# Kernel optimization log

Hardware: AMD Instinct MI355X
Metric: run time of the kernel (lower is better)

The kernel has to match this reference:

```python
import jax, jax.numpy as jnp
import numpy as np

EMBED_DIM = 256
NUM_HEADS = 8
HEAD_DIM = EMBED_DIM // NUM_HEADS


def setup_inputs() -> dict:
    key0 = jax.random.key(0)
    ks = jax.random.split(key0, 12)
    B, T, S, E = 4, 256, 16384, EMBED_DIM
    inv = 1.0 / np.sqrt(E)
    inputs = {
        "query": jax.random.normal(ks[0], (B, T, E), dtype=jnp.float32),
        "key": jax.random.normal(ks[1], (B, S, E), dtype=jnp.float32),
        "value": jax.random.normal(ks[2], (B, S, E), dtype=jnp.float32),
        "mask": jax.random.uniform(ks[3], (B, T, S), dtype=jnp.float32),
        # nn.MultiheadAttention in-projection (split into q/k/v parts) and out-projection
        "Wq": jax.random.uniform(ks[4], (E, E), jnp.float32, -inv, inv),
        "bq": jnp.zeros((E,), jnp.float32),
        "Wk": jax.random.uniform(ks[5], (E, E), jnp.float32, -inv, inv),
        "bk": jnp.zeros((E,), jnp.float32),
        "Wv": jax.random.uniform(ks[6], (E, E), jnp.float32, -inv, inv),
        "bv": jnp.zeros((E,), jnp.float32),
        "Wo": jax.random.uniform(ks[7], (E, E), jnp.float32, -inv, inv),
        "bo": jnp.zeros((E,), jnp.float32),
        # fixed default scaling factors (num_heads must be 8)
        "scaling_factors": jnp.asarray([32.0, 32.0, 16.0, 16.0, 8.0, 8.0, 4.0, 4.0], jnp.float32),
    }
    return inputs


def reference(query, key, value, mask, Wq, bq, Wk, bk, Wv, bv, Wo, bo, scaling_factors):
    B, T, E = query.shape
    S = key.shape[1]
    H, D = NUM_HEADS, HEAD_DIM
    # input projections (torch Linear convention: x @ W.T + b)
    q = (query @ Wq.T + bq).reshape(B, T, H, D).transpose(0, 2, 1, 3)  # [B,H,T,D]
    k = (key @ Wk.T + bk).reshape(B, S, H, D).transpose(0, 2, 1, 3)    # [B,H,S,D]
    v = (value @ Wv.T + bv).reshape(B, S, H, D).transpose(0, 2, 1, 3)  # [B,H,S,D]
    scale = 1.0 / jnp.sqrt(jnp.asarray(D, query.dtype))
    scores = jnp.einsum("bhtd,bhsd->bhts", q * scale, k)               # [B,H,T,S]
    # per-head scaled soft mask added as attention bias
    bias = mask[:, None, :, :] * scaling_factors[None, :, None, None]  # [B,H,T,S]
    attn = jax.nn.softmax(scores + bias, axis=-1)
    out = jnp.einsum("bhts,bhsd->bhtd", attn, v)                       # [B,H,T,D]
    out = out.transpose(0, 2, 1, 3).reshape(B, T, E)
    return out @ Wo.T + bo
```

## Files before the change

kernel.cpp:

```cpp
#include <hip/hip_runtime.h>

#define B_ 4
#define T_ 256
#define S_ 16384
#define E_ 256
#define H_ 8
#define D_ 32

typedef _Float16 f16;
typedef _Float16 f16x2 __attribute__((ext_vector_type(2)));
typedef _Float16 f16x4 __attribute__((ext_vector_type(4)));
typedef _Float16 f16x8 __attribute__((ext_vector_type(8)));
typedef float f32x4 __attribute__((ext_vector_type(4)));

typedef const __attribute__((address_space(1))) void* gas_t;
typedef __attribute__((address_space(3))) void* las_t;

#define FENCE() asm volatile("" ::: "memory")

__device__ __forceinline__ void gload_lds16(const void* g, void* l) {
    __builtin_amdgcn_global_load_lds((gas_t)g, (las_t)l, 16, 0, 0);
}

__device__ __forceinline__ f16x2 cvt_pk_f16(float a, float b) {
    return __builtin_bit_cast(f16x2, __builtin_amdgcn_cvt_pkrtz(a, b));
}

__device__ __forceinline__ f16x8 pack8(float4 a, float4 b) {
    f16x2 p0 = cvt_pk_f16(a.x, a.y), p1 = cvt_pk_f16(a.z, a.w);
    f16x2 p2 = cvt_pk_f16(b.x, b.y), p3 = cvt_pk_f16(b.z, b.w);
    return (f16x8){p0[0], p0[1], p1[0], p1[1], p2[0], p2[1], p3[0], p3[1]};
}

#define LOG2E 1.4426950408889634f

__global__ void cvt_w2_kernel(const float* __restrict__ wa, const float* __restrict__ wb,
                              f16* __restrict__ oa, f16* __restrict__ ob) {
    int m = blockIdx.y;
    const float* src = m == 0 ? wa : wb;
    f16* dst = m == 0 ? oa : ob;
    int i = (blockIdx.x * 256 + threadIdx.x) * 4;
    float4 v = *(const float4*)(src + i);
    f16x4 h = {(f16)v.x, (f16)v.y, (f16)v.z, (f16)v.w};
    *(f16x4*)(dst + i) = h;
}

template <bool OUT16>
__device__ __forceinline__ void qproj32_body(
    f16* SMEM, const float* __restrict__ in, const float* __restrict__ w,
    const float* __restrict__ bias, void* __restrict__ outp, int bid, float oscale)
{
    f16 (*As)[264] = (f16(*)[264])SMEM;
    f16 (*Bs)[264] = (f16(*)[264])(SMEM + 32 * 264);
    int tid = threadIdx.x;
    int wq = tid >> 6, ln = tid & 63, g = ln >> 4, lc = ln & 15;
    int row0 = (bid & 31) * 32;
    int n0 = (bid >> 5) * 32;
    {
        int r = tid >> 3, q0 = (tid & 7) * 32;
        const float* ip = in + (size_t)(row0 + r) * 256 + q0;
        #pragma unroll
        for (int i = 0; i < 4; i++) {
            float4 v0 = *(const float4*)(ip + i * 8);
            float4 v1 = *(const float4*)(ip + i * 8 + 4);
            *(f16x8*)&As[r][q0 + i * 8] = pack8(v0, v1);
        }
        const float* wp = w + (size_t)(n0 + r) * 256 + q0;
        #pragma unroll
        for (int i = 0; i < 4; i++) {
            float4 v0 = *(const float4*)(wp + i * 8);
            float4 v1 = *(const float4*)(wp + i * 8 + 4);
            *(f16x8*)&Bs[r][q0 + i * 8] = pack8(v0, v1);
        }
    }
    __syncthreads();
    int mi = wq >> 1, ni = wq & 1;
    f32x4 acc = {0.f, 0.f, 0.f, 0.f};
    #pragma unroll
    for (int ks = 0; ks < 8; ks++) {
        f16x8 a = *(const f16x8*)&As[mi * 16 + lc][ks * 32 + g * 8];
        f16x8 bf = *(const f16x8*)&Bs[ni * 16 + lc][ks * 32 + g * 8];
        acc = __builtin_amdgcn_mfma_f32_16x16x32_f16(a, bf, acc, 0, 0, 0);
    }
    int n = n0 + ni * 16 + lc;
    float bv = bias[n];
    #pragma unroll
    for (int r = 0; r < 4; r++) {
        int row = row0 + mi * 16 + g * 4 + r;
        float val = (acc[r] + bv) * oscale;
        if (OUT16) ((f16*)outp)[(size_t)row * 256 + n] = (f16)val;
        else       ((float*)outp)[(size_t)row * 256 + n] = val;
    }
}

template <int MODE>
__device__ __forceinline__ void proj_body4(
    char* SMEM, const float* __restrict__ in, const f16* __restrict__ w16,
    const float* __restrict__ bias, f16* __restrict__ out, int bx, float oscale)
{
    f16 (*As)[64][40] = (f16(*)[64][40])SMEM;
    f16* Bs = (f16*)(SMEM + 10240);
    int tid = threadIdx.x;
    int wv = tid >> 6, ln = tid & 63, g = ln >> 4, lc = ln & 15;
    int row0 = bx * 64;

    f32x4 acc[4][4];
    #pragma unroll
    for (int i = 0; i < 4; i++)
        #pragma unroll
        for (int j = 0; j < 4; j++) acc[i][j] = (f32x4){0.f, 0.f, 0.f, 0.f};

    int am = tid >> 3, akq = (tid & 7) << 2;
    const float* abase = in + (size_t)(row0 + am) * 256 + akq;

    float4 Ar[2][2];
    auto issueA = [&](int t) {
        const float* p = abase + t * 32;
        Ar[t & 1][0] = *(const float4*)p;
        Ar[t & 1][1] = *(const float4*)(p + (size_t)32 * 256);
    };
    auto wrA = [&](int t) {
        float4 v0 = Ar[t & 1][0], v1 = Ar[t & 1][1];
        f16x4 h0 = {(f16)v0.x, (f16)v0.y, (f16)v0.z, (f16)v0.w};
        f16x4 h1 = {(f16)v1.x, (f16)v1.y, (f16)v1.z, (f16)v1.w};
        *(f16x4*)&As[t & 1][am][akq] = h0;
        *(f16x4*)&As[t & 1][am + 32][akq] = h1;
    };
    auto issueB = [&](int t) {
        int kb = t * 32;
        #pragma unroll
        for (int c4 = 0; c4 < 4; c4++) {
            int cc = wv * 4 + c4;
            int row = cc * 16 + (ln >> 2);
            int sj = (ln & 3) ^ ((row >> 1) & 3);
            gload_lds16(w16 + (size_t)row * 256 + kb + sj * 8,
                        (char*)Bs + (t & 1) * 16384 + cc * 1024);
        }
    };

    issueB(0);
    FENCE();
    issueA(0); issueA(1);
    FENCE();

    #pragma unroll
    for (int t = 0; t < 8; t++) {
        if (t < 7) { asm volatile("s_waitcnt vmcnt(2)" ::: "memory"); }
        else       { asm volatile("s_waitcnt vmcnt(0)" ::: "memory"); }
        wrA(t);
        asm volatile("s_waitcnt lgkmcnt(0)" ::: "memory");
        __builtin_amdgcn_s_barrier();
        FENCE();
        if (t + 1 < 8) { issueB(t + 1); FENCE(); }
        if (t + 2 < 8) { issueA(t + 2); FENCE(); }

        f16x8 af[4], bf[4];
        #pragma unroll
        for (int mi = 0; mi < 4; mi++) af[mi] = *(const f16x8*)&As[t & 1][mi * 16 + lc][g * 8];
        #pragma unroll
        for (int ni = 0; ni < 4; ni++) {
            int n = wv * 64 + ni * 16 + lc;
            bf[ni] = *(const f16x8*)&Bs[(t & 1) * 8192 + n * 32 + ((g ^ ((n >> 1) & 3)) << 3)];
        }
        #pragma unroll
        for (int mi = 0; mi < 4; mi++)
            #pragma unroll
            for (int ni = 0; ni < 4; ni++)
                acc[mi][ni] = __builtin_amdgcn_mfma_f32_16x16x32_f16(af[mi], bf[ni], acc[mi][ni], 0, 0, 0);
    }

    if (MODE == 1) {
        #pragma unroll
        for (int ni = 0; ni < 4; ni++) {
            int n = wv * 64 + ni * 16 + lc;
            float bv = bias[n];
            #pragma unroll
            for (int mi = 0; mi < 4; mi++) {
                #pragma unroll
                for (int r = 0; r < 4; r++) {
                    int row = row0 + mi * 16 + g * 4 + r;
                    out[(size_t)row * 256 + n] = (f16)((acc[mi][ni][r] + bv) * oscale);
                }
            }
        }
    } else {
        f16* TR = (f16*)SMEM;
        __syncthreads();
        #pragma unroll
        for (int ni = 0; ni < 4; ni++) {
            int n = wv * 64 + ni * 16 + lc;
            float bv = bias[n];
            #pragma unroll
            for (int mi = 0; mi < 4; mi++) {
                f16x4 hv;
                #pragma unroll
                for (int r = 0; r < 4; r++) hv[r] = (f16)((acc[mi][ni][r] + bv) * oscale);
                *(f16x4*)&TR[n * 68 + mi * 16 + g * 4] = hv;
            }
        }
        __syncthreads();
        int bb = row0 >> 14, sbase = row0 & 16383;
        #pragma unroll
        for (int p = 0; p < 4; p++) {
            int n = p * 64 + wv * 16 + (ln >> 2);
            int sc = (ln & 3) * 16;
            f16x8 v0 = *(const f16x8*)&TR[n * 68 + sc];
            f16x8 v1 = *(const f16x8*)&TR[n * 68 + sc + 8];
            f16* op = out + ((size_t)(bb * 256 + n)) * 16384 + sbase + sc;
            *(f16x8*)op = v0;
            *(f16x8*)(op + 8) = v1;
        }
    }
}

__global__ __launch_bounds__(256, 3) void proj_fused4(
    const float* __restrict__ query, const float* __restrict__ key, const float* __restrict__ value,
    const float* __restrict__ Wq, const f16* __restrict__ Wk16, const f16* __restrict__ Wv16,
    const float* __restrict__ bq, const float* __restrict__ bk, const float* __restrict__ bv,
    f16* __restrict__ q16, f16* __restrict__ k16, f16* __restrict__ v16T, float qscale)
{
    __shared__ __align__(16) char SMEM[43008];
    int bx = blockIdx.x;
    if (bx < 1024) {
        proj_body4<1>(SMEM, key, Wk16, bk, k16, bx, 1.0f);
    } else if (bx < 2048) {
        proj_body4<2>(SMEM, value, Wv16, bv, v16T, bx - 1024, 1.0f);
    } else {
        qproj32_body<true>((f16*)SMEM, query, Wq, bq, q16, bx - 2048, qscale);
    }
}

__global__ __launch_bounds__(256, 4) void out_proj(
    const float* __restrict__ in, const float* __restrict__ w,
    const float* __restrict__ bias, float* __restrict__ outp)
{
    __shared__ __align__(16) f16 SMEM[16896];
    qproj32_body<false>(SMEM, in, w, bias, outp, blockIdx.x + blockIdx.y * 32, 1.0f);
}

__global__ __launch_bounds__(1024, 4) void attn_kernel(
    const f16* __restrict__ q16,
    const f16* __restrict__ k16,
    const f16* __restrict__ v16T,
    const float* __restrict__ mask,
    const float* __restrict__ scal,
    float* __restrict__ partO, float* __restrict__ partL)
{
    constexpr int ITERS = 16;
    __shared__ __align__(16) f16 KT[3][32 * 256];
    __shared__ __align__(16) f16 VT[3][256 * 32];
    __shared__ __align__(16) float MT[3][128 * 32];

    int raw = blockIdx.x;
    int th = raw >> 7, b = (raw >> 5) & 3, ck = raw & 31;
    int tid = threadIdx.x;
    int wv = tid >> 6;
    int h = wv & 7, tsub = wv >> 3;
    int ln = tid & 63, g = ln >> 4, lc = ln & 15;
    int t0 = th * 128, s0 = ck * 512;

    float sc_h = scal[h] * LOG2E;
    float negfix = -(sc_h + 4.0f);

    f16x8 qf[4];
    #pragma unroll
    for (int tl = 0; tl < 4; tl++) {
        const f16* qp = q16 + (size_t)(b * T_ + t0 + tsub * 64 + tl * 16 + lc) * E_ + h * 32 + g * 8;
        qf[tl] = *(const f16x8*)qp;
    }

    f32x4 oac[4][2];
    float l_part[4];
    #pragma unroll
    for (int tl = 0; tl < 4; tl++) {
        oac[tl][0] = (f32x4){0.f, 0.f, 0.f, 0.f};
        oac[tl][1] = (f32x4){0.f, 0.f, 0.f, 0.f};
        l_part[tl] = 0.f;
    }

    auto stage = [&](int it, int bufi) {
        int sg0 = s0 + it * 32;
        {
            int sl = wv * 2 + (ln >> 5);
            int slot = (sl ^ (sl >> 3)) & 7;
            int jc = (ln & 31) ^ slot;
            gload_lds16(k16 + (size_t)(b * S_ + sg0 + sl) * E_ + jc * 8,
                        (char*)&KT[bufi][0] + wv * 1024);
        }
        {
            int dl = wv * 16 + (ln >> 2);
            int srcj = (ln & 3) ^ ((dl >> 1) & 3);
            gload_lds16(v16T + (size_t)(b * E_ + dl) * S_ + sg0 + srcj * 8,
                        (char*)&VT[bufi][0] + wv * 1024);
        }
        {
            int r = ln >> 3;
            int sj = (ln & 7) ^ r;
            gload_lds16(mask + (size_t)(b * T_ + t0 + wv * 8 + r) * S_ + sg0 + sj * 4,
                        (char*)&MT[bufi][0] + wv * 1024);
        }
    };

    stage(0, 0);
    stage(1, 1);

    f32x4 zero4 = {0.f, 0.f, 0.f, 0.f};
    int ib = 0;

    #pragma unroll 1
    for (int it = 0; it < ITERS; it++) {
        if (it + 1 < ITERS) { asm volatile("s_waitcnt vmcnt(3)" ::: "memory"); }
        else                { asm volatile("s_waitcnt vmcnt(0)" ::: "memory"); }
        __builtin_amdgcn_s_barrier();
        FENCE();
        if (it + 2 < ITERS) {
            int wb = ib + 2; if (wb >= 3) wb -= 3;
            stage(it + 2, wb);
        }

        f16x8 kb[2];
        #pragma unroll
        for (int si = 0; si < 2; si++) {
            int sl = si * 16 + lc;
            int slot = (sl ^ (sl >> 3)) & 7;
            int j = (h * 4 + g) ^ slot;
            kb[si] = *(const f16x8*)((char*)&KT[ib][0] + sl * 512 + j * 16);
        }
        f16x4 va[2][2];
        #pragma unroll
        for (int si = 0; si < 2; si++) {
            #pragma unroll
            for (int ni = 0; ni < 2; ni++) {
                int d = h * 32 + ni * 16 + lc;
                int u = (si * 2 + (g >> 1)) ^ ((d >> 1) & 3);
                va[si][ni] = *(const f16x4*)((char*)&VT[ib][0] + d * 64 + u * 16 + (g & 1) * 8);
            }
        }

        #pragma unroll
        for (int tl = 0; tl < 4; tl++) {
            int t = tsub * 64 + tl * 16 + lc;
            const float4 mf0 = *(const float4*)((char*)&MT[ib][0] + t * 128 + (((g    ) ^ (t & 7)) << 4));
            const float4 mf1 = *(const float4*)((char*)&MT[ib][0] + t * 128 + (((4 + g) ^ (t & 7)) << 4));
            f32x4 st0 = __builtin_amdgcn_mfma_f32_16x16x32_f16(kb[0], qf[tl], zero4, 0, 0, 0);
            f32x4 st1 = __builtin_amdgcn_mfma_f32_16x16x32_f16(kb[1], qf[tl], zero4, 0, 0, 0);
            float p0 = __builtin_amdgcn_exp2f(st0[0] + __builtin_fmaf(mf0.x, sc_h, negfix));
            float p1 = __builtin_amdgcn_exp2f(st0[1] + __builtin_fmaf(mf0.y, sc_h, negfix));
            float p2 = __builtin_amdgcn_exp2f(st0[2] + __builtin_fmaf(mf0.z, sc_h, negfix));
            float p3 = __builtin_amdgcn_exp2f(st0[3] + __builtin_fmaf(mf0.w, sc_h, negfix));
            float p4 = __builtin_amdgcn_exp2f(st1[0] + __builtin_fmaf(mf1.x, sc_h, negfix));
            float p5 = __builtin_amdgcn_exp2f(st1[1] + __builtin_fmaf(mf1.y, sc_h, negfix));
            float p6 = __builtin_amdgcn_exp2f(st1[2] + __builtin_fmaf(mf1.z, sc_h, negfix));
            float p7 = __builtin_amdgcn_exp2f(st1[3] + __builtin_fmaf(mf1.w, sc_h, negfix));
            l_part[tl] += ((p0 + p1) + (p2 + p3)) + ((p4 + p5) + (p6 + p7));
            f16x2 c01 = cvt_pk_f16(p0, p1);
            f16x2 c23 = cvt_pk_f16(p2, p3);
            f16x2 c45 = cvt_pk_f16(p4, p5);
            f16x2 c67 = cvt_pk_f16(p6, p7);
            f16x4 pb0 = {c01[0], c01[1], c23[0], c23[1]};
            f16x4 pb1 = {c45[0], c45[1], c67[0], c67[1]};
            oac[tl][0] = __builtin_amdgcn_mfma_f32_16x16x16f16(va[0][0], pb0, oac[tl][0], 0, 0, 0);
            oac[tl][0] = __builtin_amdgcn_mfma_f32_16x16x16f16(va[1][0], pb1, oac[tl][0], 0, 0, 0);
            oac[tl][1] = __builtin_amdgcn_mfma_f32_16x16x16f16(va[0][1], pb0, oac[tl][1], 0, 0, 0);
            oac[tl][1] = __builtin_amdgcn_mfma_f32_16x16x16f16(va[1][1], pb1, oac[tl][1], 0, 0, 0);
        }
        ib++; if (ib >= 3) ib -= 3;
    }

    #pragma unroll
    for (int tl = 0; tl < 4; tl++) {
        float lv = l_part[tl];
        lv += __shfl_xor(lv, 16, 64);
        lv += __shfl_xor(lv, 32, 64);
        l_part[tl] = lv;
    }
    float* po = partO + (size_t)raw * 128 * 256;
    #pragma unroll
    for (int tl = 0; tl < 4; tl++) {
        #pragma unroll
        for (int ni = 0; ni < 2; ni++) {
            float4 o4 = {oac[tl][ni][0], oac[tl][ni][1], oac[tl][ni][2], oac[tl][ni][3]};
            *(float4*)(po + (size_t)(tsub * 64 + tl * 16 + lc) * 256 + h * 32 + ni * 16 + g * 4) = o4;
        }
    }
    if (g == 0) {
        float* pl = partL + (size_t)raw * 128 * 8;
        #pragma unroll
        for (int tl = 0; tl < 4; tl++) {
            int trow = tsub * 64 + tl * 16 + lc;
            pl[trow * 8 + h] = l_part[tl];
        }
    }
}

__global__ __launch_bounds__(256) void combine_kernel(
    const float* __restrict__ partO, const float* __restrict__ partL,
    float* __restrict__ attnO)
{
    int bid = blockIdx.x;
    int b = bid >> 8, t = bid & 255;
    int th = t >> 7, tl = t & 127;
    int tid = threadIdx.x;
    __shared__ float sl[32][8];
    {
        int ck = tid >> 3, hh = tid & 7;
        size_t blk = (size_t)(th * 128 + b * 32 + ck);
        sl[ck][hh] = partL[blk * 1024 + tl * 8 + hh];
    }
    __syncthreads();
    int h = tid >> 5;
    float L = 0.f;
    #pragma unroll 8
    for (int ck = 0; ck < 32; ck++) L += sl[ck][h];
    float acc = 0.f;
    #pragma unroll 4
    for (int ck = 0; ck < 32; ck++) {
        size_t blk = (size_t)(th * 128 + b * 32 + ck);
        acc += partO[blk * 32768 + (size_t)tl * 256 + tid];
    }
    attnO[(size_t)bid * 256 + tid] = acc / L;
}

extern "C" void kernel_launch(void* const* d_in, const int* in_sizes, int n_in,
                              void* d_out, int out_size, void* d_ws, size_t ws_size,
                              hipStream_t stream) {
    (void)in_sizes; (void)n_in; (void)out_size; (void)ws_size;
    const float* query = (const float*)d_in[0];
    const float* key   = (const float*)d_in[1];
    const float* value = (const float*)d_in[2];
    const float* mask  = (const float*)d_in[3];
    const float* Wq = (const float*)d_in[4];
    const float* bq = (const float*)d_in[5];
    const float* Wk = (const float*)d_in[6];
    const float* bk = (const float*)d_in[7];
    const float* Wv = (const float*)d_in[8];
    const float* bv = (const float*)d_in[9];
    const float* Wo = (const float*)d_in[10];
    const float* bo = (const float*)d_in[11];
    const float* scal = (const float*)d_in[12];

    char* ws = (char*)d_ws;
    f16* Wk16 = (f16*)(ws + 0);
    f16* Wv16 = (f16*)(ws + (1 << 17));
    f16* q16  = (f16*)(ws + (4 << 17));
    float* attnO = (float*)(ws + 1048576);
    f16* k16  = (f16*)(ws + 2097152);
    f16* v16T = (f16*)(ws + 35651584);
    float* partO = (float*)(ws + 69206016);
    float* partL = (float*)(ws + 103809024);

    cvt_w2_kernel<<<dim3(64, 2), 256, 0, stream>>>(Wk, Wv, Wk16, Wv16);

    const float qscale = 0.17677669529663687f * LOG2E;
    proj_fused4<<<2304, 256, 0, stream>>>(query, key, value, Wq, Wk16, Wv16,
                                          bq, bk, bv, q16, k16, v16T, qscale);

    attn_kernel<<<256, 1024, 0, stream>>>(q16, k16, v16T, mask, scal, partO, partL);
    combine_kernel<<<1024, 256, 0, stream>>>(partO, partL, attnO);

    out_proj<<<dim3(32, 8), 256, 0, stream>>>(attnO, Wo, bo, (float*)d_out);
}
```

Baseline: 127.3 us.

## Restructure K/V projection to 512-thread blocks with full A-tile preload

The K/V projection is rewritten to use 512-thread blocks. Each block loads the whole 64x256 fp32 input tile into LDS as f16 up front, and each wave owns a private 32-column slice of the weight tile, which removes the per-step block barrier and double buffering. The weight conversion and Q projection are merged into one pre-kernel, which removes a launch. The trade-off is more LDS per block and a single-buffered weight stream that can expose load latency.

```diff
diff --git a/kernel.cpp b/kernel.cpp
--- a/kernel.cpp
+++ b/kernel.cpp
@@ -33,17 +33,6 @@
 }
 
 #define LOG2E 1.4426950408889634f
-
-__global__ void cvt_w2_kernel(const float* __restrict__ wa, const float* __restrict__ wb,
-                              f16* __restrict__ oa, f16* __restrict__ ob) {
-    int m = blockIdx.y;
-    const float* src = m == 0 ? wa : wb;
-    f16* dst = m == 0 ? oa : ob;
-    int i = (blockIdx.x * 256 + threadIdx.x) * 4;
-    float4 v = *(const float4*)(src + i);
-    f16x4 h = {(f16)v.x, (f16)v.y, (f16)v.z, (f16)v.w};
-    *(f16x4*)(dst + i) = h;
-}
 
 template <bool OUT16>
 __device__ __forceinline__ void qproj32_body(
@@ -93,86 +82,99 @@
     }
 }
 
+__global__ __launch_bounds__(256) void pre_kernel(
+    const float* __restrict__ Wk, const float* __restrict__ Wv,
+    f16* __restrict__ Wk16, f16* __restrict__ Wv16,
+    const float* __restrict__ query, const float* __restrict__ Wq,
+    const float* __restrict__ bq, f16* __restrict__ q16, float qscale)
+{
+    __shared__ __align__(16) f16 SMEM[16896];
+    int bx = blockIdx.x;
+    if (bx < 128) {
+        const float* src = bx < 64 ? Wk : Wv;
+        f16* dst = bx < 64 ? Wk16 : Wv16;
+        int i = ((bx & 63) * 256 + threadIdx.x) * 4;
+        float4 v = *(const float4*)(src + i);
+        f16x4 h = {(f16)v.x, (f16)v.y, (f16)v.z, (f16)v.w};
+        *(f16x4*)(dst + i) = h;
+    } else {
+        qproj32_body<true>(SMEM, query, Wq, bq, q16, bx - 128, qscale);
+    }
+}
+
 template <int MODE>
-__device__ __forceinline__ void proj_body4(
+__device__ __forceinline__ void proj_body6(
     char* SMEM, const float* __restrict__ in, const f16* __restrict__ w16,
     const float* __restrict__ bias, f16* __restrict__ out, int bx, float oscale)
 {
-    f16 (*As)[64][40] = (f16(*)[64][40])SMEM;
-    f16* Bs = (f16*)(SMEM + 10240);
+    f16* As = (f16*)SMEM;
+    f16* Bs = (f16*)(SMEM + 33280);
     int tid = threadIdx.x;
-    int wv = tid >> 6, ln = tid & 63, g = ln >> 4, lc = ln & 15;
+    int wq = tid >> 6, ln = tid & 63, g = ln >> 4, lc = ln & 15;
     int row0 = bx * 64;
 
-    f32x4 acc[4][4];
-    #pragma unroll
-    for (int i = 0; i < 4; i++)
-        #pragma unroll
-        for (int j = 0; j < 4; j++) acc[i][j] = (f32x4){0.f, 0.f, 0.f, 0.f};
-
-    int am = tid >> 3, akq = (tid & 7) << 2;
-    const float* abase = in + (size_t)(row0 + am) * 256 + akq;
-
-    float4 Ar[2][2];
-    auto issueA = [&](int t) {
-        const float* p = abase + t * 32;
-        Ar[t & 1][0] = *(const float4*)p;
-        Ar[t & 1][1] = *(const float4*)(p + (size_t)32 * 256);
-    };
-    auto wrA = [&](int t) {
-        float4 v0 = Ar[t & 1][0], v1 = Ar[t & 1][1];
-        f16x4 h0 = {(f16)v0.x, (f16)v0.y, (f16)v0.z, (f16)v0.w};
-        f16x4 h1 = {(f16)v1.x, (f16)v1.y, (f16)v1.z, (f16)v1.w};
-        *(f16x4*)&As[t & 1][am][akq] = h0;
-        *(f16x4*)&As[t & 1][am + 32][akq] = h1;
-    };
     auto issueB = [&](int t) {
         int kb = t * 32;
         #pragma unroll
-        for (int c4 = 0; c4 < 4; c4++) {
-            int cc = wv * 4 + c4;
-            int row = cc * 16 + (ln >> 2);
+        for (int hh = 0; hh < 2; hh++) {
+            int row = wq * 32 + hh * 16 + (ln >> 2);
             int sj = (ln & 3) ^ ((row >> 1) & 3);
             gload_lds16(w16 + (size_t)row * 256 + kb + sj * 8,
-                        (char*)Bs + (t & 1) * 16384 + cc * 1024);
+                        (char*)Bs + (wq * 32 + hh * 16) * 64);
         }
     };
 
     issueB(0);
     FENCE();
-    issueA(0); issueA(1);
-    FENCE();
+    const float* ab = in + (size_t)row0 * 256;
+    f32x4 Ld[8];
+    #pragma unroll
+    for (int j = 0; j < 8; j++)
+        Ld[j] = *(const f32x4*)(ab + (size_t)j * 2048 + tid * 4);
+    asm volatile("s_waitcnt vmcnt(0)" ::: "memory");
+    #pragma unroll
+    for (int j = 0; j < 8; j++) {
+        int row = j * 8 + wq;
+        f16x4 h = {(f16)Ld[j][0], (f16)Ld[j][1], (f16)Ld[j][2], (f16)Ld[j][3]};
+        *(f16x4*)&As[row * 260 + ln * 4] = h;
+    }
+    __syncthreads();
+
+    f32x4 acc[4][2];
+    #pragma unroll
+    for (int i = 0; i < 4; i++) {
+        acc[i][0] = (f32x4){0.f, 0.f, 0.f, 0.f};
+        acc[i][1] = (f32x4){0.f, 0.f, 0.f, 0.f};
+    }
 
     #pragma unroll
     for (int t = 0; t < 8; t++) {
-        if (t < 7) { asm volatile("s_waitcnt vmcnt(2)" ::: "memory"); }
-        else       { asm volatile("s_waitcnt vmcnt(0)" ::: "memory"); }
-        wrA(t);
+        asm volatile("s_waitcnt vmcnt(0)" ::: "memory");
+        FENCE();
+        f16x8 bf[2];
+        #pragma unroll
+        for (int ni = 0; ni < 2; ni++) {
+            int n = wq * 32 + ni * 16 + lc;
+            bf[ni] = *(const f16x8*)&Bs[n * 32 + ((g ^ ((n >> 1) & 3)) << 3)];
+        }
         asm volatile("s_waitcnt lgkmcnt(0)" ::: "memory");
-        __builtin_amdgcn_s_barrier();
         FENCE();
         if (t + 1 < 8) { issueB(t + 1); FENCE(); }
-        if (t + 2 < 8) { issueA(t + 2); FENCE(); }
-
-        f16x8 af[4], bf[4];
-        #pragma unroll
-        for (int mi = 0; mi < 4; mi++) af[mi] = *(const f16x8*)&As[t & 1][mi * 16 + lc][g * 8];
-        #pragma unroll
-        for (int ni = 0; ni < 4; ni++) {
-            int n = wv * 64 + ni * 16 + lc;
-            bf[ni] = *(const f16x8*)&Bs[(t & 1) * 8192 + n * 32 + ((g ^ ((n >> 1) & 3)) << 3)];
-        }
+        f16x8 af[4];
         #pragma unroll
         for (int mi = 0; mi < 4; mi++)
-            #pragma unroll
-            for (int ni = 0; ni < 4; ni++)
-                acc[mi][ni] = __builtin_amdgcn_mfma_f32_16x16x32_f16(af[mi], bf[ni], acc[mi][ni], 0, 0, 0);
+            af[mi] = *(const f16x8*)&As[(mi * 16 + lc) * 260 + t * 32 + g * 8];
+        #pragma unroll
+        for (int mi = 0; mi < 4; mi++) {
+            acc[mi][0] = __builtin_amdgcn_mfma_f32_16x16x32_f16(af[mi], bf[0], acc[mi][0], 0, 0, 0);
+            acc[mi][1] = __builtin_amdgcn_mfma_f32_16x16x32_f16(af[mi], bf[1], acc[mi][1], 0, 0, 0);
+        }
     }
 
     if (MODE == 1) {
         #pragma unroll
-        for (int ni = 0; ni < 4; ni++) {
-            int n = wv * 64 + ni * 16 + lc;
+        for (int ni = 0; ni < 2; ni++) {
+            int n = wq * 32 + ni * 16 + lc;
             float bv = bias[n];
             #pragma unroll
             for (int mi = 0; mi < 4; mi++) {
@@ -187,8 +189,8 @@
         f16* TR = (f16*)SMEM;
         __syncthreads();
         #pragma unroll
-        for (int ni = 0; ni < 4; ni++) {
-            int n = wv * 64 + ni * 16 + lc;
+        for (int ni = 0; ni < 2; ni++) {
+            int n = wq * 32 + ni * 16 + lc;
             float bv = bias[n];
             #pragma unroll
             for (int mi = 0; mi < 4; mi++) {
@@ -201,8 +203,8 @@
         __syncthreads();
         int bb = row0 >> 14, sbase = row0 & 16383;
         #pragma unroll
-        for (int p = 0; p < 4; p++) {
-            int n = p * 64 + wv * 16 + (ln >> 2);
+        for (int p = 0; p < 2; p++) {
+            int n = p * 128 + wq * 16 + (ln >> 2);
             int sc = (ln & 3) * 16;
             f16x8 v0 = *(const f16x8*)&TR[n * 68 + sc];
             f16x8 v1 = *(const f16x8*)&TR[n * 68 + sc + 8];
@@ -213,21 +215,16 @@
     }
 }
 
-__global__ __launch_bounds__(256, 3) void proj_fused4(
-    const float* __restrict__ query, const float* __restrict__ key, const float* __restrict__ value,
-    const float* __restrict__ Wq, const f16* __restrict__ Wk16, const f16* __restrict__ Wv16,
-    const float* __restrict__ bq, const float* __restrict__ bk, const float* __restrict__ bv,
-    f16* __restrict__ q16, f16* __restrict__ k16, f16* __restrict__ v16T, float qscale)
-{
-    __shared__ __align__(16) char SMEM[43008];
+__global__ __launch_bounds__(512, 4) void proj_kv6(
+    const float* __restrict__ key, const float* __restrict__ value,
+    const f16* __restrict__ Wk16, const f16* __restrict__ Wv16,
+    const float* __restrict__ bk, const float* __restrict__ bv,
+    f16* __restrict__ k16, f16* __restrict__ v16T)
+{
+    __shared__ __align__(16) char SMEM[49664];
     int bx = blockIdx.x;
-    if (bx < 1024) {
-        proj_body4<1>(SMEM, key, Wk16, bk, k16, bx, 1.0f);
-    } else if (bx < 2048) {
-        proj_body4<2>(SMEM, value, Wv16, bv, v16T, bx - 1024, 1.0f);
-    } else {
-        qproj32_body<true>((f16*)SMEM, query, Wq, bq, q16, bx - 2048, qscale);
-    }
+    if (bx < 1024) proj_body6<1>(SMEM, key,   Wk16, bk, k16,  bx, 1.0f);
+    else           proj_body6<2>(SMEM, value, Wv16, bv, v16T, bx - 1024, 1.0f);
 }
 
 __global__ __launch_bounds__(256, 4) void out_proj(
@@ -449,11 +446,10 @@
     float* partO = (float*)(ws + 69206016);
     float* partL = (float*)(ws + 103809024);
 
-    cvt_w2_kernel<<<dim3(64, 2), 256, 0, stream>>>(Wk, Wv, Wk16, Wv16);
-
     const float qscale = 0.17677669529663687f * LOG2E;
-    proj_fused4<<<2304, 256, 0, stream>>>(query, key, value, Wq, Wk16, Wv16,
-                                          bq, bk, bv, q16, k16, v16T, qscale);
+    pre_kernel<<<384, 256, 0, stream>>>(Wk, Wv, Wk16, Wv16, query, Wq, bq, q16, qscale);
+
+    proj_kv6<<<2048, 512, 0, stream>>>(key, value, Wk16, Wv16, bk, bv, k16, v16T);
 
     attn_kernel<<<256, 1024, 0, stream>>>(q16, k16, v16T, mask, scal, partO, partL);
     combine_kernel<<<1024, 256, 0, stream>>>(partO, partL, attnO);
```

Result: slower. 145.2 us (+14.1%).

## Stream fp32 activations directly into LDS with triple-buffered async loads

Applied to the files above, without the earlier changes.

The K/V projection now loads the fp32 activation tiles straight into LDS with global_load_lds (XOR-swizzled) instead of going through registers, and converts to fp16 when reading fragments from LDS. Staging becomes a three-buffer ring with a two-tile lookahead and a single barrier per step. The aim is to remove register staging and the LDS write/lgkm wait from the critical path and overlap more memory traffic. In exchange, LDS use grows to 72KB and occupancy drops from 3 to 2 blocks per CU.

```diff
diff --git a/kernel.cpp b/kernel.cpp
--- a/kernel.cpp
+++ b/kernel.cpp
@@ -29,6 +29,12 @@
 __device__ __forceinline__ f16x8 pack8(float4 a, float4 b) {
     f16x2 p0 = cvt_pk_f16(a.x, a.y), p1 = cvt_pk_f16(a.z, a.w);
     f16x2 p2 = cvt_pk_f16(b.x, b.y), p3 = cvt_pk_f16(b.z, b.w);
+    return (f16x8){p0[0], p0[1], p1[0], p1[1], p2[0], p2[1], p3[0], p3[1]};
+}
+
+__device__ __forceinline__ f16x8 pack8v(f32x4 a, f32x4 b) {
+    f16x2 p0 = cvt_pk_f16(a[0], a[1]), p1 = cvt_pk_f16(a[2], a[3]);
+    f16x2 p2 = cvt_pk_f16(b[0], b[1]), p3 = cvt_pk_f16(b[2], b[3]);
     return (f16x8){p0[0], p0[1], p1[0], p1[1], p2[0], p2[1], p3[0], p3[1]};
 }
 
@@ -94,79 +100,77 @@
 }
 
 template <int MODE>
-__device__ __forceinline__ void proj_body4(
+__device__ __forceinline__ void proj_body7(
     char* SMEM, const float* __restrict__ in, const f16* __restrict__ w16,
     const float* __restrict__ bias, f16* __restrict__ out, int bx, float oscale)
 {
-    f16 (*As)[64][40] = (f16(*)[64][40])SMEM;
-    f16* Bs = (f16*)(SMEM + 10240);
+    char* Ab = SMEM;
+    char* Bb = SMEM + 24576;
     int tid = threadIdx.x;
     int wv = tid >> 6, ln = tid & 63, g = ln >> 4, lc = ln & 15;
     int row0 = bx * 64;
 
-    f32x4 acc[4][4];
-    #pragma unroll
-    for (int i = 0; i < 4; i++)
-        #pragma unroll
-        for (int j = 0; j < 4; j++) acc[i][j] = (f32x4){0.f, 0.f, 0.f, 0.f};
-
-    int am = tid >> 3, akq = (tid & 7) << 2;
-    const float* abase = in + (size_t)(row0 + am) * 256 + akq;
-
-    float4 Ar[2][2];
-    auto issueA = [&](int t) {
-        const float* p = abase + t * 32;
-        Ar[t & 1][0] = *(const float4*)p;
-        Ar[t & 1][1] = *(const float4*)(p + (size_t)32 * 256);
-    };
-    auto wrA = [&](int t) {
-        float4 v0 = Ar[t & 1][0], v1 = Ar[t & 1][1];
-        f16x4 h0 = {(f16)v0.x, (f16)v0.y, (f16)v0.z, (f16)v0.w};
-        f16x4 h1 = {(f16)v1.x, (f16)v1.y, (f16)v1.z, (f16)v1.w};
-        *(f16x4*)&As[t & 1][am][akq] = h0;
-        *(f16x4*)&As[t & 1][am + 32][akq] = h1;
-    };
-    auto issueB = [&](int t) {
-        int kb = t * 32;
+    auto stage = [&](int t, int buf) {
         #pragma unroll
         for (int c4 = 0; c4 < 4; c4++) {
             int cc = wv * 4 + c4;
             int row = cc * 16 + (ln >> 2);
             int sj = (ln & 3) ^ ((row >> 1) & 3);
-            gload_lds16(w16 + (size_t)row * 256 + kb + sj * 8,
-                        (char*)Bs + (t & 1) * 16384 + cc * 1024);
+            gload_lds16(w16 + (size_t)row * 256 + t * 32 + sj * 8,
+                        Bb + buf * 16384 + cc * 1024);
+        }
+        #pragma unroll
+        for (int q2 = 0; q2 < 2; q2++) {
+            int q = wv * 2 + q2;
+            int rl = ln >> 3;
+            int ssl = (ln & 7) ^ rl;
+            gload_lds16(in + (size_t)(row0 + q * 8 + rl) * 256 + t * 32 + ssl * 4,
+                        Ab + buf * 8192 + q * 1024);
         }
     };
 
-    issueB(0);
-    FENCE();
-    issueA(0); issueA(1);
-    FENCE();
-
-    #pragma unroll
+    f32x4 acc[4][4];
+    #pragma unroll
+    for (int i = 0; i < 4; i++)
+        #pragma unroll
+        for (int j = 0; j < 4; j++) acc[i][j] = (f32x4){0.f, 0.f, 0.f, 0.f};
+
+    stage(0, 0);
+    stage(1, 1);
+
+    int ib = 0;
+    #pragma unroll 1
     for (int t = 0; t < 8; t++) {
-        if (t < 7) { asm volatile("s_waitcnt vmcnt(2)" ::: "memory"); }
+        if (t < 7) { asm volatile("s_waitcnt vmcnt(6)" ::: "memory"); }
         else       { asm volatile("s_waitcnt vmcnt(0)" ::: "memory"); }
-        wrA(t);
-        asm volatile("s_waitcnt lgkmcnt(0)" ::: "memory");
         __builtin_amdgcn_s_barrier();
         FENCE();
-        if (t + 1 < 8) { issueB(t + 1); FENCE(); }
-        if (t + 2 < 8) { issueA(t + 2); FENCE(); }
+        if (t + 2 < 8) {
+            int wb = ib + 2; if (wb >= 3) wb -= 3;
+            stage(t + 2, wb);
+        }
 
         f16x8 af[4], bf[4];
         #pragma unroll
-        for (int mi = 0; mi < 4; mi++) af[mi] = *(const f16x8*)&As[t & 1][mi * 16 + lc][g * 8];
+        for (int mi = 0; mi < 4; mi++) {
+            int row = mi * 16 + lc;
+            int s0 = (2 * g) ^ (row & 7);
+            int s1 = (2 * g + 1) ^ (row & 7);
+            f32x4 lo = *(const f32x4*)(Ab + ib * 8192 + row * 128 + s0 * 16);
+            f32x4 hi = *(const f32x4*)(Ab + ib * 8192 + row * 128 + s1 * 16);
+            af[mi] = pack8v(lo, hi);
+        }
         #pragma unroll
         for (int ni = 0; ni < 4; ni++) {
             int n = wv * 64 + ni * 16 + lc;
-            bf[ni] = *(const f16x8*)&Bs[(t & 1) * 8192 + n * 32 + ((g ^ ((n >> 1) & 3)) << 3)];
+            bf[ni] = *(const f16x8*)(Bb + ib * 16384 + n * 64 + ((g ^ ((n >> 1) & 3)) << 4));
         }
         #pragma unroll
         for (int mi = 0; mi < 4; mi++)
             #pragma unroll
             for (int ni = 0; ni < 4; ni++)
                 acc[mi][ni] = __builtin_amdgcn_mfma_f32_16x16x32_f16(af[mi], bf[ni], acc[mi][ni], 0, 0, 0);
+        ib++; if (ib >= 3) ib -= 3;
     }
 
     if (MODE == 1) {
@@ -213,18 +217,18 @@
     }
 }
 
-__global__ __launch_bounds__(256, 3) void proj_fused4(
+__global__ __launch_bounds__(256, 2) void proj_fused7(
     const float* __restrict__ query, const float* __restrict__ key, const float* __restrict__ value,
     const float* __restrict__ Wq, const f16* __restrict__ Wk16, const f16* __restrict__ Wv16,
     const float* __restrict__ bq, const float* __restrict__ bk, const float* __restrict__ bv,
     f16* __restrict__ q16, f16* __restrict__ k16, f16* __restrict__ v16T, float qscale)
 {
-    __shared__ __align__(16) char SMEM[43008];
+    __shared__ __align__(16) char SMEM[73728];
     int bx = blockIdx.x;
     if (bx < 1024) {
-        proj_body4<1>(SMEM, key, Wk16, bk, k16, bx, 1.0f);
+        proj_body7<1>(SMEM, key, Wk16, bk, k16, bx, 1.0f);
     } else if (bx < 2048) {
-        proj_body4<2>(SMEM, value, Wv16, bv, v16T, bx - 1024, 1.0f);
+        proj_body7<2>(SMEM, value, Wv16, bv, v16T, bx - 1024, 1.0f);
     } else {
         qproj32_body<true>((f16*)SMEM, query, Wq, bq, q16, bx - 2048, qscale);
     }
@@ -452,7 +456,7 @@
     cvt_w2_kernel<<<dim3(64, 2), 256, 0, stream>>>(Wk, Wv, Wk16, Wv16);
 
     const float qscale = 0.17677669529663687f * LOG2E;
-    proj_fused4<<<2304, 256, 0, stream>>>(query, key, value, Wq, Wk16, Wv16,
+    proj_fused7<<<2304, 256, 0, stream>>>(query, key, value, Wq, Wk16, Wv16,
                                           bq, bk, bv, q16, k16, v16T, qscale);
 
     attn_kernel<<<256, 1024, 0, stream>>>(q16, k16, v16T, mask, scal, partO, partL);
```

Result: no change. 126.7 us, median of 2 (-0.4%).

## Enlarge K/V projection tiles to 128 rows and move Q projection into pre-kernel

Applied to the files above, without the earlier changes.

The K/V projection moves to a new 512-thread kernel that computes 128-row tiles with 8 waves, so each loaded weight tile serves twice as many rows. A-tile loads become contiguous 8-element chunks packed in one store. The K output is now staged through LDS for coalesced row writes. The Q projection is folded into the weight-conversion pre-kernel, which removes a launch and takes Q blocks out of the big projection grid. The costs are more LDS per block, lower occupancy (2 blocks of 512 threads), and extra barriers in the two-pass epilogue.

```diff
diff --git a/kernel.cpp b/kernel.cpp
--- a/kernel.cpp
+++ b/kernel.cpp
@@ -33,17 +33,6 @@
 }
 
 #define LOG2E 1.4426950408889634f
-
-__global__ void cvt_w2_kernel(const float* __restrict__ wa, const float* __restrict__ wb,
-                              f16* __restrict__ oa, f16* __restrict__ ob) {
-    int m = blockIdx.y;
-    const float* src = m == 0 ? wa : wb;
-    f16* dst = m == 0 ? oa : ob;
-    int i = (blockIdx.x * 256 + threadIdx.x) * 4;
-    float4 v = *(const float4*)(src + i);
-    f16x4 h = {(f16)v.x, (f16)v.y, (f16)v.z, (f16)v.w};
-    *(f16x4*)(dst + i) = h;
-}
 
 template <bool OUT16>
 __device__ __forceinline__ void qproj32_body(
@@ -93,16 +82,37 @@
     }
 }
 
+__global__ __launch_bounds__(256) void pre_kernel(
+    const float* __restrict__ Wk, const float* __restrict__ Wv,
+    f16* __restrict__ Wk16, f16* __restrict__ Wv16,
+    const float* __restrict__ query, const float* __restrict__ Wq,
+    const float* __restrict__ bq, f16* __restrict__ q16, float qscale)
+{
+    __shared__ __align__(16) f16 SMEM[16896];
+    int bx = blockIdx.x;
+    if (bx < 128) {
+        const float* src = bx < 64 ? Wk : Wv;
+        f16* dst = bx < 64 ? Wk16 : Wv16;
+        int i = ((bx & 63) * 256 + threadIdx.x) * 4;
+        float4 v = *(const float4*)(src + i);
+        f16x4 h = {(f16)v.x, (f16)v.y, (f16)v.z, (f16)v.w};
+        *(f16x4*)(dst + i) = h;
+    } else {
+        qproj32_body<true>(SMEM, query, Wq, bq, q16, bx - 128, qscale);
+    }
+}
+
 template <int MODE>
-__device__ __forceinline__ void proj_body4(
+__device__ __forceinline__ void proj8_body(
     char* SMEM, const float* __restrict__ in, const f16* __restrict__ w16,
-    const float* __restrict__ bias, f16* __restrict__ out, int bx, float oscale)
-{
-    f16 (*As)[64][40] = (f16(*)[64][40])SMEM;
-    f16* Bs = (f16*)(SMEM + 10240);
+    const float* __restrict__ bias, f16* __restrict__ out, int bx)
+{
+    f16 (*As)[128][40] = (f16(*)[128][40])SMEM;
+    f16* Bs = (f16*)(SMEM + 20480);
     int tid = threadIdx.x;
-    int wv = tid >> 6, ln = tid & 63, g = ln >> 4, lc = ln & 15;
-    int row0 = bx * 64;
+    int wq = tid >> 6, ln = tid & 63, g = ln >> 4, lc = ln & 15;
+    int mh = wq >> 2, nq = wq & 3;
+    int row0 = bx * 128;
 
     f32x4 acc[4][4];
     #pragma unroll
@@ -110,27 +120,23 @@
         #pragma unroll
         for (int j = 0; j < 4; j++) acc[i][j] = (f32x4){0.f, 0.f, 0.f, 0.f};
 
-    int am = tid >> 3, akq = (tid & 7) << 2;
+    int am = tid >> 2, akq = (tid & 3) << 3;
     const float* abase = in + (size_t)(row0 + am) * 256 + akq;
 
     float4 Ar[2][2];
     auto issueA = [&](int t) {
         const float* p = abase + t * 32;
         Ar[t & 1][0] = *(const float4*)p;
-        Ar[t & 1][1] = *(const float4*)(p + (size_t)32 * 256);
+        Ar[t & 1][1] = *(const float4*)(p + 4);
     };
     auto wrA = [&](int t) {
-        float4 v0 = Ar[t & 1][0], v1 = Ar[t & 1][1];
-        f16x4 h0 = {(f16)v0.x, (f16)v0.y, (f16)v0.z, (f16)v0.w};
-        f16x4 h1 = {(f16)v1.x, (f16)v1.y, (f16)v1.z, (f16)v1.w};
-        *(f16x4*)&As[t & 1][am][akq] = h0;
-        *(f16x4*)&As[t & 1][am + 32][akq] = h1;
+        *(f16x8*)&As[t & 1][am][akq] = pack8(Ar[t & 1][0], Ar[t & 1][1]);
     };
     auto issueB = [&](int t) {
         int kb = t * 32;
         #pragma unroll
-        for (int c4 = 0; c4 < 4; c4++) {
-            int cc = wv * 4 + c4;
+        for (int c2 = 0; c2 < 2; c2++) {
+            int cc = wq * 2 + c2;
             int row = cc * 16 + (ln >> 2);
             int sj = (ln & 3) ^ ((row >> 1) & 3);
             gload_lds16(w16 + (size_t)row * 256 + kb + sj * 8,
@@ -156,10 +162,11 @@
 
         f16x8 af[4], bf[4];
         #pragma unroll
-        for (int mi = 0; mi < 4; mi++) af[mi] = *(const f16x8*)&As[t & 1][mi * 16 + lc][g * 8];
+        for (int mi = 0; mi < 4; mi++)
+            af[mi] = *(const f16x8*)&As[t & 1][mh * 64 + mi * 16 + lc][g * 8];
         #pragma unroll
         for (int ni = 0; ni < 4; ni++) {
-            int n = wv * 64 + ni * 16 + lc;
+            int n = nq * 64 + ni * 16 + lc;
             bf[ni] = *(const f16x8*)&Bs[(t & 1) * 8192 + n * 32 + ((g ^ ((n >> 1) & 3)) << 3)];
         }
         #pragma unroll
@@ -170,64 +177,69 @@
     }
 
     if (MODE == 1) {
-        #pragma unroll
-        for (int ni = 0; ni < 4; ni++) {
-            int n = wv * 64 + ni * 16 + lc;
-            float bv = bias[n];
-            #pragma unroll
-            for (int mi = 0; mi < 4; mi++) {
+        f16 (*TR)[264] = (f16(*)[264])SMEM;
+        #pragma unroll
+        for (int p = 0; p < 2; p++) {
+            __syncthreads();
+            if (mh == p) {
                 #pragma unroll
-                for (int r = 0; r < 4; r++) {
-                    int row = row0 + mi * 16 + g * 4 + r;
-                    out[(size_t)row * 256 + n] = (f16)((acc[mi][ni][r] + bv) * oscale);
+                for (int ni = 0; ni < 4; ni++) {
+                    int n = nq * 64 + ni * 16 + lc;
+                    float bv = bias[n];
+                    #pragma unroll
+                    for (int mi = 0; mi < 4; mi++)
+                        #pragma unroll
+                        for (int r = 0; r < 4; r++)
+                            TR[mi * 16 + g * 4 + r][n] = (f16)(acc[mi][ni][r] + bv);
                 }
             }
+            __syncthreads();
+            int r = tid >> 3, c = tid & 7;
+            f16* op = out + (size_t)(row0 + p * 64 + r) * 256 + c * 32;
+            #pragma unroll
+            for (int i = 0; i < 4; i++)
+                *(f16x8*)(op + i * 8) = *(const f16x8*)&TR[r][c * 32 + i * 8];
         }
     } else {
-        f16* TR = (f16*)SMEM;
-        __syncthreads();
-        #pragma unroll
-        for (int ni = 0; ni < 4; ni++) {
-            int n = wv * 64 + ni * 16 + lc;
-            float bv = bias[n];
+        f16 (*TR)[68] = (f16(*)[68])SMEM;
+        int bb = row0 >> 14, sbase = row0 & 16383;
+        #pragma unroll
+        for (int p = 0; p < 2; p++) {
+            __syncthreads();
+            if (mh == p) {
+                #pragma unroll
+                for (int ni = 0; ni < 4; ni++) {
+                    int n = nq * 64 + ni * 16 + lc;
+                    float bv = bias[n];
+                    #pragma unroll
+                    for (int mi = 0; mi < 4; mi++) {
+                        f16x4 hv;
+                        #pragma unroll
+                        for (int r = 0; r < 4; r++) hv[r] = (f16)(acc[mi][ni][r] + bv);
+                        *(f16x4*)&TR[n][mi * 16 + g * 4] = hv;
+                    }
+                }
+            }
+            __syncthreads();
+            int n = tid >> 1, hf = tid & 1;
+            f16* op = out + (((size_t)(bb * 256 + n)) << 14) + sbase + p * 64 + hf * 32;
             #pragma unroll
-            for (int mi = 0; mi < 4; mi++) {
-                f16x4 hv;
-                #pragma unroll
-                for (int r = 0; r < 4; r++) hv[r] = (f16)((acc[mi][ni][r] + bv) * oscale);
-                *(f16x4*)&TR[n * 68 + mi * 16 + g * 4] = hv;
-            }
-        }
-        __syncthreads();
-        int bb = row0 >> 14, sbase = row0 & 16383;
-        #pragma unroll
-        for (int p = 0; p < 4; p++) {
-            int n = p * 64 + wv * 16 + (ln >> 2);
-            int sc = (ln & 3) * 16;
-            f16x8 v0 = *(const f16x8*)&TR[n * 68 + sc];
-            f16x8 v1 = *(const f16x8*)&TR[n * 68 + sc + 8];
-            f16* op = out + ((size_t)(bb * 256 + n)) * 16384 + sbase + sc;
-            *(f16x8*)op = v0;
-            *(f16x8*)(op + 8) = v1;
-        }
-    }
-}
-
-__global__ __launch_bounds__(256, 3) void proj_fused4(
-    const float* __restrict__ query, const float* __restrict__ key, const float* __restrict__ value,
-    const float* __restrict__ Wq, const f16* __restrict__ Wk16, const f16* __restrict__ Wv16,
-    const float* __restrict__ bq, const float* __restrict__ bk, const float* __restrict__ bv,
-    f16* __restrict__ q16, f16* __restrict__ k16, f16* __restrict__ v16T, float qscale)
-{
-    __shared__ __align__(16) char SMEM[43008];
+            for (int i = 0; i < 4; i++)
+                *(f16x8*)(op + i * 8) = *(const f16x8*)&TR[n][hf * 32 + i * 8];
+        }
+    }
+}
+
+__global__ __launch_bounds__(512, 2) void proj_kv8(
+    const float* __restrict__ key, const float* __restrict__ value,
+    const f16* __restrict__ Wk16, const f16* __restrict__ Wv16,
+    const float* __restrict__ bk, const float* __restrict__ bv,
+    f16* __restrict__ k16, f16* __restrict__ v16T)
+{
+    __shared__ __align__(16) char SMEM[53248];
     int bx = blockIdx.x;
-    if (bx < 1024) {
-        proj_body4<1>(SMEM, key, Wk16, bk, k16, bx, 1.0f);
-    } else if (bx < 2048) {
-        proj_body4<2>(SMEM, value, Wv16, bv, v16T, bx - 1024, 1.0f);
-    } else {
-        qproj32_body<true>((f16*)SMEM, query, Wq, bq, q16, bx - 2048, qscale);
-    }
+    if (bx < 512) proj8_body<1>(SMEM, key,   Wk16, bk, k16,  bx);
+    else          proj8_body<2>(SMEM, value, Wv16, bv, v16T, bx - 512);
 }
 
 __global__ __launch_bounds__(256, 4) void out_proj(
@@ -449,11 +461,10 @@
     float* partO = (float*)(ws + 69206016);
     float* partL = (float*)(ws + 103809024);
 
-    cvt_w2_kernel<<<dim3(64, 2), 256, 0, stream>>>(Wk, Wv, Wk16, Wv16);
-
     const float qscale = 0.17677669529663687f * LOG2E;
-    proj_fused4<<<2304, 256, 0, stream>>>(query, key, value, Wq, Wk16, Wv16,
-                                          bq, bk, bv, q16, k16, v16T, qscale);
+    pre_kernel<<<384, 256, 0, stream>>>(Wk, Wv, Wk16, Wv16, query, Wq, bq, q16, qscale);
+
+    proj_kv8<<<1024, 512, 0, stream>>>(key, value, Wk16, Wv16, bk, bv, k16, v16T);
 
     attn_kernel<<<256, 1024, 0, stream>>>(q16, k16, v16T, mask, scal, partO, partL);
     combine_kernel<<<1024, 256, 0, stream>>>(partO, partL, attnO);
```

New measurement: 135.6 us. 6.6% more time.
